# Performance work log

Measured on AMD Instinct MI355X. Metric: run time of the kernel, lower is better.

## Reference

```python
import jax, jax.numpy as jnp
import numpy as np

# Config (matches init_kwargs)
T, B = 128, 32
I, H, O, G = 128, 320, 32, 8
GROUP = 16  # attn_group_size entries, 8 groups of 16 -> sums to I
DT, TAU_X, TAU_W = 0.02, 0.1, 0.2
ALPHA_X = DT / TAU_X          # 0.2
ALPHA_W = DT / TAU_W          # 0.1
E_PROP = 0.8


def _masks():
    e_h = int(E_PROP * H)  # 256
    # x2h: e_prop=1, zero_cols_prop=0, no diag removal -> all ones
    mask_x = jnp.ones((H, I), dtype=jnp.float32)
    # h2h: sign mask (+1 for E, -1 for I), diagonal zeroed
    sign_h = jnp.concatenate([jnp.ones(e_h), -jnp.ones(H - e_h)]).astype(jnp.float32)
    mask_h = jnp.tile(sign_h[None, :], (H, 1)) * (1.0 - jnp.eye(H, dtype=jnp.float32))
    # h2o: zero_cols = int(0.2*H) trailing columns removed, sign mask on the rest
    zc = int((1.0 - E_PROP) * H)  # 64
    exist = jnp.concatenate([jnp.ones(H - zc), jnp.zeros(zc)]).astype(jnp.float32)
    mask_o = jnp.tile((sign_h * exist)[None, :], (O, 1))
    # attn EILinear(H -> G): same column pattern as h2o
    mask_a = jnp.tile((sign_h * exist)[None, :], (G, 1))
    return mask_x, mask_h, mask_o, mask_a


def setup_inputs() -> dict:
    key = jax.random.key(0)
    ks = jax.random.split(key, 10)
    s = 0.05  # keep dynamics in a sane range
    return {
        "x": jax.random.normal(ks[0], (T, B, I), dtype=jnp.float32),
        "Rs": jax.random.uniform(ks[1], (T, B, 1), dtype=jnp.float32),
        "W_x2h": jax.random.normal(ks[2], (H, I), dtype=jnp.float32) * s,
        "W_h2h": jax.random.normal(ks[3], (H, H), dtype=jnp.float32) * s,
        "b_h2h": jax.random.normal(ks[4], (H,), dtype=jnp.float32) * s,
        "W_h2o": jax.random.normal(ks[5], (O, H), dtype=jnp.float32) * s,
        "b_h2o": jax.random.normal(ks[6], (O,), dtype=jnp.float32) * s,
        "W_attn": jax.random.normal(ks[7], (G, H), dtype=jnp.float32) * s,
        "b_attn": jax.random.normal(ks[8], (G,), dtype=jnp.float32) * s,
        "c_plas": jax.random.normal(ks[9], (6,), dtype=jnp.float32) * s,
    }


def reference(x, Rs, W_x2h, W_h2h, b_h2h, W_h2o, b_h2o, W_attn, b_attn, c_plas):
    mask_x, mask_h, mask_o, mask_a = _masks()
    relu = jax.nn.relu
    # effective (sign/existence constrained, positive) weights
    ew_attn = relu(W_attn) * mask_a                      # [G, H]
    ew_x0 = relu(W_x2h) * mask_x                         # [H, I]
    ew_h0 = relu(W_h2h) * mask_h                         # [H, H]
    c = jnp.abs(c_plas)

    state0 = jnp.zeros((B, H), dtype=x.dtype)            # x0=0, sigma_rec=0
    output0 = relu(state0)
    wx0 = jnp.broadcast_to(ew_x0[None], (B, H, I))       # batched fast weights
    wh0 = jnp.broadcast_to(ew_h0[None], (B, H, H))

    def step(carry, inp):
        state, output, wx, wh = carry
        x_t, R_t = inp                                   # [B,I], [B,1]
        # attention over hidden groups
        attn = jax.nn.softmax(output @ ew_attn.T + b_attn, axis=-1)  # [B,G]
        attn_full = jnp.repeat(attn, GROUP, axis=-1)     # [B,I]
        xm = x_t * attn_full * G
        # masked / positive-constrained fast weights applied per batch
        ewx = relu(wx) * mask_x[None]                    # [B,H,I]
        ewh = relu(wh) * mask_h[None]                    # [B,H,H]
        total = (jnp.einsum('bhi,bi->bh', ewx, xm)
                 + jnp.einsum('bhj,bj->bh', ewh, output) + b_h2h)
        new_state = state * (1.0 - ALPHA_X) + total * ALPHA_X
        new_output = jnp.tanh(relu(new_state))           # retanh
        # outer-product plasticity update
        R = R_t[:, :, None]                              # [B,1,1]
        wx_n = wx * (1.0 - ALPHA_W) + ALPHA_W * R * (
            c[0] * xm[:, None, :]
            + c[1] * new_output[:, :, None]
            + c[2] * jnp.einsum('bi,bj->bij', new_output, xm))
        wh_n = wh * (1.0 - ALPHA_W) + ALPHA_W * R * (
            c[3] * output[:, None, :]
            + c[4] * new_output[:, :, None]
            + c[5] * jnp.einsum('bi,bj->bij', new_output, output))
        return (new_state, new_output, wx_n, wh_n), new_output

    _, hs = jax.lax.scan(step, (state0, output0, wx0, wh0), (x, Rs))  # hs: [T,B,H]
    ew_o = relu(W_h2o) * mask_o                          # [O,H]
    out = jax.nn.sigmoid(jnp.einsum('tbh,oh->tbo', hs, ew_o) + b_h2o)
    return out, hs
```

## Files before the change

kernel.cpp:

```cpp
#include <hip/hip_runtime.h>

#define TT 128
#define BB 32
#define II 128
#define HH 320
#define OO 32
#define GG 8
#define HPAD 129

static __device__ __forceinline__ float fexp2(float x) { return __builtin_amdgcn_exp2f(x); }
static __device__ __forceinline__ float frcp(float x)  { return __builtin_amdgcn_rcpf(x); }

static __device__ __forceinline__ float tanh_pos(float x) {
    float e = fexp2(x * 2.8853900817779268f);
    return 1.0f - 2.0f * frcp(e + 1.0f);
}

__global__ __launch_bounds__(512, 2)
void leaky_rnn_kernel(const float* __restrict__ x, const float* __restrict__ Rs,
                      const float* __restrict__ Wx2h, const float* __restrict__ Wh2h,
                      const float* __restrict__ bh2h, const float* __restrict__ Wh2o,
                      const float* __restrict__ bh2o, const float* __restrict__ Wattn,
                      const float* __restrict__ battn, const float* __restrict__ cplas,
                      float* __restrict__ out, float* __restrict__ hs,
                      unsigned* __restrict__ ctr)
{
    const int tid  = threadIdx.x;
    const int bid  = blockIdx.x;
    const int b    = bid >> 3;
    const int sub  = bid & 7;
    const int w    = tid >> 6;
    const int lane = tid & 63;
    const int h0   = sub * 40;

    __shared__ float s_ea[GG * HH];
    __shared__ float s_out[HH];
    __shared__ float s_xm[II];
    __shared__ float s_logit[GG];
    __shared__ float s_hist[40 * HPAD];
    __shared__ float s_hs[16 * HH];

    for (int idx = tid; idx < GG * HH; idx += 512) {
        int h = idx % HH;
        float m = (h < 256) ? 1.f : (h == 256 ? -1.f : 0.f);
        s_ea[idx] = fmaxf(Wattn[idx], 0.f) * m;
    }
    if (tid < HH) s_out[tid] = 0.f;

    float wx[5][2], wh[5][5], st[5], bh[5];
    int hrow[5];
#pragma unroll
    for (int r = 0; r < 5; ++r) {
        int h = h0 + w * 5 + r;
        hrow[r] = h;
        bh[r] = bh2h[h];
        st[r] = 0.f;
#pragma unroll
        for (int c = 0; c < 2; ++c)
            wx[r][c] = fmaxf(Wx2h[h * II + lane + 64 * c], 0.f);
#pragma unroll
        for (int c = 0; c < 5; ++c) {
            int j = lane + 64 * c;
            float v = fmaxf(Wh2h[h * HH + j], 0.f);
            v = (c == 4) ? -v : v;
            wh[r][c] = (j == h) ? 0.f : v;
        }
    }
    float batt = battn[w];
    float c0 = fabsf(cplas[0]), c1 = fabsf(cplas[1]), c2 = fabsf(cplas[2]);
    float c3 = fabsf(cplas[3]), c4 = fabsf(cplas[4]), c5 = fabsf(cplas[5]);

    const float AX  = (float)(0.02 / 0.1);
    const float AW  = (float)(0.02 / 0.2);
    const float OMX = 1.f - AX;
    const float OMW = 1.f - AW;
    const float L2E = 1.4426950408889634f;

    __syncthreads();

    float xv_next = (tid < II) ? x[b * II + tid] : 0.f;

#pragma unroll 1
    for (int t = 0; t < TT; ++t) {
        float xv = xv_next;
        float Rv = Rs[t * BB + b];
        float A  = AW * Rv;

        float lp = 0.f;
#pragma unroll
        for (int k = 0; k < 5; ++k) {
            int hh2 = lane + 64 * k;
            lp = fmaf(s_ea[w * HH + hh2], s_out[hh2], lp);
        }
#pragma unroll
        for (int m = 1; m < 64; m <<= 1) lp += __shfl_xor(lp, m, 64);
        if (lane == 0) s_logit[w] = lp + batt;
        __syncthreads();

        if (tid < II) {
            float lg[8];
#pragma unroll
            for (int g = 0; g < 8; ++g) lg[g] = s_logit[g];
            float mx = lg[0];
#pragma unroll
            for (int g = 1; g < 8; ++g) mx = fmaxf(mx, lg[g]);
            float se = 0.f, eg[8];
#pragma unroll
            for (int g = 0; g < 8; ++g) { eg[g] = fexp2((lg[g] - mx) * L2E); se += eg[g]; }
            s_xm[tid] = xv * eg[tid >> 4] * 8.f * frcp(se);
        }
        __syncthreads();

        float xmc0 = s_xm[lane], xmc1 = s_xm[lane + 64];
        float oc[5];
#pragma unroll
        for (int c = 0; c < 5; ++c) oc[c] = s_out[lane + 64 * c];

        float no[5];
#pragma unroll
        for (int r = 0; r < 5; ++r) {
            int h = hrow[r];
            float p = fmaxf(wx[r][0], 0.f) * xmc0;
            p = fmaf(fmaxf(wx[r][1], 0.f), xmc1, p);
#pragma unroll
            for (int c = 0; c < 5; ++c) {
                float wv = fmaxf(wh[r][c], 0.f);
                float so = (c == 4) ? -oc[4] : oc[c];
                float term = wv * so;
                term = ((lane + 64 * c) == h) ? 0.f : term;
                p += term;
            }
#pragma unroll
            for (int m = 1; m < 64; m <<= 1) p += __shfl_xor(p, m, 64);
            float total = p + bh[r];
            st[r] = fmaf(st[r], OMX, total * AX);
            no[r] = tanh_pos(fmaxf(st[r], 0.f));
            if (lane == r) {
                __hip_atomic_store(&hs[(t * BB + b) * HH + h], no[r] + 2.0f,
                                   __ATOMIC_RELAXED, __HIP_MEMORY_SCOPE_AGENT);
                s_hist[(w * 5 + r) * HPAD + t] = no[r];
            }
        }

        if (t < TT - 1) {
            float Ac0 = A * c0, Ac1 = A * c1, Ac2 = A * c2;
            float Ac3 = A * c3, Ac4 = A * c4, Ac5 = A * c5;
#pragma unroll
            for (int r = 0; r < 5; ++r) {
                float u  = fmaf(Ac2, no[r], Ac0);
                float v  = Ac1 * no[r];
                float pp = fmaf(Ac5, no[r], Ac3);
                float qq = Ac4 * no[r];
                wx[r][0] = fmaf(wx[r][0], OMW, fmaf(u, xmc0, v));
                wx[r][1] = fmaf(wx[r][1], OMW, fmaf(u, xmc1, v));
#pragma unroll
                for (int c = 0; c < 5; ++c)
                    wh[r][c] = fmaf(wh[r][c], OMW, fmaf(pp, oc[c], qq));
            }
        }

        if (t + 1 < TT)
            xv_next = (tid < II) ? x[((t + 1) * BB + b) * II + tid] : 0.f;

        __syncthreads();

        if (t < TT - 1 && tid < HH) {
            float v;
            if (tid >= h0 && tid < h0 + 40) {
                v = s_hist[(tid - h0) * HPAD + t];
            } else {
                int guard = 0;
                do {
                    v = __hip_atomic_load(&hs[(t * BB + b) * HH + tid],
                                          __ATOMIC_RELAXED, __HIP_MEMORY_SCOPE_AGENT);
                    if (++guard > 2000000) break;
                } while (v < 1.0f);
                v -= 2.0f;
            }
            s_out[tid] = v;
        }
        __syncthreads();
    }

    if (tid == 0) {
        __hip_atomic_fetch_add(&ctr[b * 32], 1u, __ATOMIC_RELAXED, __HIP_MEMORY_SCOPE_AGENT);
        int guard = 0;
        while (__hip_atomic_load(&ctr[b * 32], __ATOMIC_RELAXED, __HIP_MEMORY_SCOPE_AGENT) < 8u) {
            if (++guard > 2000000) break;
            __builtin_amdgcn_s_sleep(1);
        }
    }
    __syncthreads();

    for (int idx = tid; idx < 16 * HH; idx += 512) {
        int tl = idx / HH, h = idx % HH;
        int t_g = sub * 16 + tl;
        s_hs[idx] = __hip_atomic_load(&hs[(t_g * BB + b) * HH + h],
                                      __ATOMIC_RELAXED, __HIP_MEMORY_SCOPE_AGENT) - 2.0f;
    }
    __syncthreads();
    {
        int t_loc = tid >> 5;
        int o     = tid & 31;
        int t_g   = sub * 16 + t_loc;
        const float* hp = &s_hs[t_loc * HH];
        float acc = bh2o[o];
#pragma unroll 4
        for (int h = 0; h < 257; ++h) {
            float m = (h == 256) ? -1.f : 1.f;
            acc = fmaf(fmaxf(Wh2o[o * HH + h], 0.f) * m, hp[h], acc);
        }
        float sg = frcp(1.f + fexp2(-acc * L2E));
        out[(t_g * BB + b) * OO + o] = sg;
    }

    __syncthreads();
    if (tid == 0) {
        __hip_atomic_fetch_add(&ctr[b * 32], 1u, __ATOMIC_RELAXED, __HIP_MEMORY_SCOPE_AGENT);
        int guard = 0;
        while (__hip_atomic_load(&ctr[b * 32], __ATOMIC_RELAXED, __HIP_MEMORY_SCOPE_AGENT) < 16u) {
            if (++guard > 2000000) break;
            __builtin_amdgcn_s_sleep(1);
        }
    }
    __syncthreads();

    for (int idx = tid; idx < 40 * TT; idx += 512) {
        int row = idx >> 7;
        int t   = idx & 127;
        __hip_atomic_store(&hs[(t * BB + b) * HH + h0 + row], s_hist[row * HPAD + t],
                           __ATOMIC_RELAXED, __HIP_MEMORY_SCOPE_AGENT);
    }
}

extern "C" void kernel_launch(void* const* d_in, const int* in_sizes, int n_in,
                              void* d_out, int out_size, void* d_ws, size_t ws_size,
                              hipStream_t stream) {
    const float* x     = (const float*)d_in[0];
    const float* Rs    = (const float*)d_in[1];
    const float* Wx2h  = (const float*)d_in[2];
    const float* Wh2h  = (const float*)d_in[3];
    const float* bh2h  = (const float*)d_in[4];
    const float* Wh2o  = (const float*)d_in[5];
    const float* bh2o  = (const float*)d_in[6];
    const float* Wattn = (const float*)d_in[7];
    const float* battn = (const float*)d_in[8];
    const float* cplas = (const float*)d_in[9];
    float* out = (float*)d_out;
    float* hs  = out + TT * BB * OO;
    unsigned* ctr = (unsigned*)d_ws;

    hipMemsetAsync(d_ws, 0, 32 * 32 * sizeof(unsigned), stream);
    hipLaunchKernelGGL(leaky_rnn_kernel, dim3(256), dim3(512), 0, stream,
                       x, Rs, Wx2h, Wh2h, bh2h, Wh2o, bh2o, Wattn, battn, cplas,
                       out, hs, ctr);
}
```

Before: 528.4 us.

## Double-buffer recurrent state, compute softmax per wave, batch shuffle reductions

Double-buffers the shared output vector so the barrier between the weight update and the next-state gather can be removed. Each wave now computes the attention softmax and its input modulation redundantly, which drops a second block barrier and the shared xm buffer. The five cross-lane shuffle reductions are interleaved to expose ILP, and own-block outputs are now read back through the global spin-load path instead of local history. This removes two block barriers per timestep but adds redundant exp work and extra global polling for locally produced values.

```diff
diff --git a/kernel.cpp b/kernel.cpp
--- a/kernel.cpp
+++ b/kernel.cpp
@@ -34,8 +34,7 @@
     const int h0   = sub * 40;
 
     __shared__ float s_ea[GG * HH];
-    __shared__ float s_out[HH];
-    __shared__ float s_xm[II];
+    __shared__ float s_out[2][HH];
     __shared__ float s_logit[GG];
     __shared__ float s_hist[40 * HPAD];
     __shared__ float s_hs[16 * HH];
@@ -45,7 +44,7 @@
         float m = (h < 256) ? 1.f : (h == 256 ? -1.f : 0.f);
         s_ea[idx] = fmaxf(Wattn[idx], 0.f) * m;
     }
-    if (tid < HH) s_out[tid] = 0.f;
+    if (tid < HH) { s_out[0][tid] = 0.f; s_out[1][tid] = 0.f; }
 
     float wx[5][2], wh[5][5], st[5], bh[5];
     int hrow[5];
@@ -78,67 +77,85 @@
 
     __syncthreads();
 
-    float xv_next = (tid < II) ? x[b * II + tid] : 0.f;
+    float xv0n = x[b * II + lane];
+    float xv1n = x[b * II + lane + 64];
+    float Rvn  = Rs[b];
 
 #pragma unroll 1
     for (int t = 0; t < TT; ++t) {
-        float xv = xv_next;
-        float Rv = Rs[t * BB + b];
-        float A  = AW * Rv;
+        const float* so_cur = s_out[t & 1];
+        float*       so_nxt = s_out[(t + 1) & 1];
+        float xv0 = xv0n, xv1 = xv1n;
+        float A   = AW * Rvn;
 
         float lp = 0.f;
 #pragma unroll
         for (int k = 0; k < 5; ++k) {
             int hh2 = lane + 64 * k;
-            lp = fmaf(s_ea[w * HH + hh2], s_out[hh2], lp);
+            lp = fmaf(s_ea[w * HH + hh2], so_cur[hh2], lp);
         }
 #pragma unroll
         for (int m = 1; m < 64; m <<= 1) lp += __shfl_xor(lp, m, 64);
         if (lane == 0) s_logit[w] = lp + batt;
         __syncthreads();
 
-        if (tid < II) {
-            float lg[8];
-#pragma unroll
-            for (int g = 0; g < 8; ++g) lg[g] = s_logit[g];
-            float mx = lg[0];
-#pragma unroll
-            for (int g = 1; g < 8; ++g) mx = fmaxf(mx, lg[g]);
-            float se = 0.f, eg[8];
-#pragma unroll
-            for (int g = 0; g < 8; ++g) { eg[g] = fexp2((lg[g] - mx) * L2E); se += eg[g]; }
-            s_xm[tid] = xv * eg[tid >> 4] * 8.f * frcp(se);
-        }
-        __syncthreads();
-
-        float xmc0 = s_xm[lane], xmc1 = s_xm[lane + 64];
+        float lg[8];
+#pragma unroll
+        for (int g = 0; g < 8; ++g) lg[g] = s_logit[g];
+        float mx = lg[0];
+#pragma unroll
+        for (int g = 1; g < 8; ++g) mx = fmaxf(mx, lg[g]);
+        float se = 0.f, eg[8];
+#pragma unroll
+        for (int g = 0; g < 8; ++g) { eg[g] = fexp2((lg[g] - mx) * L2E); se += eg[g]; }
+        float rinv = frcp(se);
+        float xmc0 = xv0 * eg[lane >> 4] * 8.f * rinv;
+        float xmc1 = xv1 * eg[(lane >> 4) + 4] * 8.f * rinv;
+
         float oc[5];
 #pragma unroll
-        for (int c = 0; c < 5; ++c) oc[c] = s_out[lane + 64 * c];
-
-        float no[5];
+        for (int c = 0; c < 5; ++c) oc[c] = so_cur[lane + 64 * c];
+
+        float p[5];
 #pragma unroll
         for (int r = 0; r < 5; ++r) {
             int h = hrow[r];
-            float p = fmaxf(wx[r][0], 0.f) * xmc0;
-            p = fmaf(fmaxf(wx[r][1], 0.f), xmc1, p);
+            float pp = fmaxf(wx[r][0], 0.f) * xmc0;
+            pp = fmaf(fmaxf(wx[r][1], 0.f), xmc1, pp);
 #pragma unroll
             for (int c = 0; c < 5; ++c) {
                 float wv = fmaxf(wh[r][c], 0.f);
                 float so = (c == 4) ? -oc[4] : oc[c];
                 float term = wv * so;
                 term = ((lane + 64 * c) == h) ? 0.f : term;
-                p += term;
+                pp += term;
             }
-#pragma unroll
-            for (int m = 1; m < 64; m <<= 1) p += __shfl_xor(p, m, 64);
-            float total = p + bh[r];
+            p[r] = pp;
+        }
+#pragma unroll
+        for (int m = 1; m < 64; m <<= 1) {
+#pragma unroll
+            for (int r = 0; r < 5; ++r) p[r] += __shfl_xor(p[r], m, 64);
+        }
+
+        float no[5];
+#pragma unroll
+        for (int r = 0; r < 5; ++r) {
+            float total = p[r] + bh[r];
             st[r] = fmaf(st[r], OMX, total * AX);
             no[r] = tanh_pos(fmaxf(st[r], 0.f));
-            if (lane == r) {
-                __hip_atomic_store(&hs[(t * BB + b) * HH + h], no[r] + 2.0f,
+        }
+
+        {
+            float pub = no[0];
+            pub = (lane == 1) ? no[1] : pub;
+            pub = (lane == 2) ? no[2] : pub;
+            pub = (lane == 3) ? no[3] : pub;
+            pub = (lane == 4) ? no[4] : pub;
+            if (lane < 5) {
+                __hip_atomic_store(&hs[(t * BB + b) * HH + h0 + w * 5 + lane], pub + 2.0f,
                                    __ATOMIC_RELAXED, __HIP_MEMORY_SCOPE_AGENT);
-                s_hist[(w * 5 + r) * HPAD + t] = no[r];
+                s_hist[(w * 5 + lane) * HPAD + t] = pub;
             }
         }
 
@@ -159,25 +176,19 @@
             }
         }
 
-        if (t + 1 < TT)
-            xv_next = (tid < II) ? x[((t + 1) * BB + b) * II + tid] : 0.f;
-
-        __syncthreads();
+        if (t + 1 < TT) {
+            xv0n = x[((t + 1) * BB + b) * II + lane];
+            xv1n = x[((t + 1) * BB + b) * II + lane + 64];
+            Rvn  = Rs[(t + 1) * BB + b];
+        }
 
         if (t < TT - 1 && tid < HH) {
-            float v;
-            if (tid >= h0 && tid < h0 + 40) {
-                v = s_hist[(tid - h0) * HPAD + t];
-            } else {
-                int guard = 0;
-                do {
-                    v = __hip_atomic_load(&hs[(t * BB + b) * HH + tid],
-                                          __ATOMIC_RELAXED, __HIP_MEMORY_SCOPE_AGENT);
-                    if (++guard > 2000000) break;
-                } while (v < 1.0f);
-                v -= 2.0f;
-            }
-            s_out[tid] = v;
+            const float* p2 = &hs[(t * BB + b) * HH + tid];
+            float v; int guard = 0;
+            do {
+                v = __hip_atomic_load(p2, __ATOMIC_RELAXED, __HIP_MEMORY_SCOPE_AGENT);
+            } while (v < 1.0f && ++guard < 2000000);
+            so_nxt[tid] = v - 2.0f;
         }
         __syncthreads();
     }
```

Result: faster. 476.7 us (-9.8%).
